# Performance work log

Measured on AMD Instinct MI355X. Metric: run time of the kernel, lower is better.

The kernel has to match this reference:

```python
import jax, jax.numpy as jnp
import numpy as np


def _u(k, shape, s):
    return jax.random.uniform(k, shape, jnp.float32, -s, s)


def setup_inputs() -> dict:
    B, T, F, H = 256, 256, 128, 256
    key = jax.random.key(0)
    ks = jax.random.split(key, 40)
    sH = 1.0 / np.sqrt(H).astype(np.float32)
    sF = 1.0 / np.sqrt(F).astype(np.float32)
    s2F = 1.0 / np.sqrt(2 * F).astype(np.float32)
    s3F = 1.0 / np.sqrt(3 * F).astype(np.float32)
    d = {
        'x': jax.random.normal(ks[0], (B, T, F), jnp.float32),
        'masking': (jax.random.uniform(ks[1], (B, T, F)) < 0.8).astype(jnp.float32),
        'time_lag': jax.random.uniform(ks[2], (B, T, F), jnp.float32),
        # forward LSTMCell (torch layout: W_ih [4H,2F], W_hh [4H,H], gates i,f,g,o)
        'fw_Wih': _u(ks[3], (4 * H, 2 * F), sH), 'fw_Whh': _u(ks[4], (4 * H, H), sH),
        'fw_bih': _u(ks[5], (4 * H,), sH), 'fw_bhh': _u(ks[6], (4 * H,), sH),
        'bw_Wih': _u(ks[7], (4 * H, 2 * F), sH), 'bw_Whh': _u(ks[8], (4 * H, H), sH),
        'bw_bih': _u(ks[9], (4 * H,), sH), 'bw_bhh': _u(ks[10], (4 * H,), sH),
        'fwlin_W': _u(ks[11], (F, H), sH), 'fwlin_b': _u(ks[12], (F,), sH),
        'bwlin_W': _u(ks[13], (F, H), sH), 'bwlin_b': _u(ks[14], (F,), sH),
        'fwz_W': _u(ks[15], (F, F), sF), 'fwz_b': _u(ks[16], (F,), sF),
        'bwz_W': _u(ks[17], (F, F), sF), 'bwz_b': _u(ks[18], (F,), sF),
        # beta linear 2F -> 3F
        'fwbeta_W': _u(ks[19], (3 * F, 2 * F), s2F), 'fwbeta_b': _u(ks[20], (3 * F,), s2F),
        'bwbeta_W': _u(ks[21], (3 * F, 2 * F), s2F), 'bwbeta_b': _u(ks[22], (3 * F,), s2F),
        # time-lag decay F -> H (both directions)
        'lag_W': _u(ks[23], (H, F), sF), 'lag_b': _u(ks[24], (H,), sF),
        'lagb_W': _u(ks[25], (H, F), sF), 'lagb_b': _u(ks[26], (H,), sF),
        # r_beta H -> F (both directions)
        'rbeta_W': _u(ks[27], (F, H), sH), 'rbeta_b': _u(ks[28], (F,), sH),
        'rbetab_W': _u(ks[29], (F, H), sH), 'rbetab_b': _u(ks[30], (F,), sH),
        # shared linear_layer_test 3F -> F
        'test_W': _u(ks[31], (F, 3 * F), s3F), 'test_b': _u(ks[32], (F,), s3F),
    }
    return d


def _lstm_cell(inp, h, c, Wih, Whh, bih, bhh):
    g = inp @ Wih.T + bih + h @ Whh.T + bhh
    i, f, gg, o = jnp.split(g, 4, axis=-1)
    c2 = jax.nn.sigmoid(f) * c + jax.nn.sigmoid(i) * jnp.tanh(gg)
    h2 = jax.nn.sigmoid(o) * jnp.tanh(c2)
    return h2, c2


def _run_dir(x, m, rr, rb, lin_W, lin_b, z_W, z_b, beta_W, beta_b, test_W, test_b, Wih, Whh, bih, bhh):
    # x, m: [T,B,F]; rr: [T,B,H]; rb: [T,B,F]
    F = x.shape[-1]
    offdiag = 1.0 - jnp.eye(F, dtype=x.dtype)

    def step(carry, inp):
        h, c = carry
        xj, mj, rj, rbj = inp
        out = h @ lin_W.T + lin_b                                 # [B,F]
        x_c = mj * xj + (1.0 - mj) * out
        z = x_c @ (z_W * offdiag).T + z_b
        beta = jax.nn.sigmoid(jnp.concatenate([mj, rbj], -1) @ beta_W.T + beta_b)
        beta = beta @ test_W.T + test_b                           # [B,F]
        c_val = beta * z + (1.0 - beta) * out
        c_c = mj * xj + (1.0 - mj) * c_val
        h2, c2 = _lstm_cell(jnp.concatenate([c_c, mj], -1), h * rj, c, Wih, Whh, bih, bhh)
        return (h2, c2), (out, z, c_val)

    bs, H = x.shape[1], Whh.shape[-1]
    h0 = jnp.zeros((bs, H), x.dtype)
    _, (outs, zs, cs) = jax.lax.scan(step, (h0, h0), (x, m, rr, rb))
    return outs, zs, cs


def reference(x, masking, time_lag, fw_Wih, fw_Whh, fw_bih, fw_bhh, bw_Wih, bw_Whh, bw_bih, bw_bhh, fwlin_W, fwlin_b, bwlin_W, bwlin_b, fwz_W, fwz_b, bwz_W, bwz_b, fwbeta_W, fwbeta_b, bwbeta_W, bwbeta_b, lag_W, lag_b, lagb_W, lagb_b, rbeta_W, rbeta_b, rbetab_W, rbetab_b, test_W, test_b):
    xt = jnp.transpose(x, (1, 0, 2))         # [T,B,F]
    mt = jnp.transpose(masking, (1, 0, 2))
    lt = jnp.transpose(time_lag, (1, 0, 2))
    # forward direction decay
    rr_f = jnp.exp(-jax.nn.relu(lt @ lag_W.T + lag_b))            # [T,B,H]
    rb_f = rr_f @ rbeta_W.T + rbeta_b                             # [T,B,F]
    of, zf, cf = _run_dir(xt, mt, rr_f, rb_f, fwlin_W, fwlin_b, fwz_W, fwz_b,
                          fwbeta_W, fwbeta_b, test_W, test_b, fw_Wih, fw_Whh, fw_bih, fw_bhh)
    # backward direction: iterate time reversed, then un-reverse outputs
    rr_b = jnp.exp(-jax.nn.relu(lt @ lagb_W.T + lagb_b))
    rb_b = rr_b @ rbetab_W.T + rbetab_b
    rev = lambda a: a[::-1]
    ob, zb, cb = _run_dir(rev(xt), rev(mt), rev(rr_b), rev(rb_b), bwlin_W, bwlin_b,
                          bwz_W, bwz_b, bwbeta_W, bwbeta_b, test_W, test_b,
                          bw_Wih, bw_Whh, bw_bih, bw_bhh)
    ob, zb, cb = rev(ob), rev(zb), rev(cb)
    perm = lambda a: jnp.transpose(a, (1, 0, 2))                  # back to [B,T,F]
    return (perm(of), perm(zf), perm(cf), perm(ob), perm(zb), perm(cb))
```

## Files before the change

kernel.cpp:

```cpp
#include <hip/hip_runtime.h>
#include <stdint.h>

#define TT 256
#define FF 128
#define HH 256
#define BB 256
#define BTc (BB * TT)
#define BTFc ((size_t)BB * TT * FF)

typedef __attribute__((ext_vector_type(8))) short short8;
typedef __attribute__((ext_vector_type(4))) float floatx4;
typedef __attribute__((ext_vector_type(4))) int intx4;

__device__ __forceinline__ floatx4 mfma16(short8 a, short8 b, floatx4 c) {
    return __builtin_amdgcn_mfma_f32_16x16x32_bf16(a, b, c, 0, 0, 0);
}
__device__ __forceinline__ intx4 mfmai8(long a, long b, intx4 c) {
    return __builtin_amdgcn_mfma_i32_16x16x32_i8(a, b, c, 0, 0, 0);
}

__device__ __forceinline__ float bf2f(short s) {
    return __uint_as_float(((unsigned)(unsigned short)s) << 16);
}
__device__ __forceinline__ short f2bf(float f) {
    unsigned u = __float_as_uint(f);
    u += 0x7FFFu + ((u >> 16) & 1u);
    return (short)(u >> 16);
}
__device__ __forceinline__ short8 ld_cvt8(const float* __restrict__ p) {
    short8 r;
#pragma unroll
    for (int j = 0; j < 8; ++j) r[j] = f2bf(p[j]);
    return r;
}
__device__ __forceinline__ float sigf(float x) { return 1.f / (1.f + __expf(-x)); }
__device__ __forceinline__ float tanhf_(float x) { return 1.f - 2.f / (1.f + __expf(2.f * x)); }

#define BARSYNC() do { asm volatile("s_waitcnt lgkmcnt(0)" ::: "memory"); \
                       __builtin_amdgcn_s_barrier(); } while (0)

struct PrepArgs {
    const float *s0, *s1, *s2, *s3, *s4, *s5, *s6;
    short *d0, *d1, *d2, *d3, *d4, *d5, *d6;
};
struct ScaleDesc { const float* src; int stride; int coloff; int K; int nrows; int sbase; };
struct ScaleArgs { ScaleDesc d[6]; float* s; };
struct PackBDesc { const float* src; short* dst; int stride; int coloff; int kts; int diag; int groups; };
struct AArgs { PrepArgs p; ScaleArgs s; PackBDesc b[6]; };

__global__ __launch_bounds__(256) void k_a(AArgs A) {
    if (blockIdx.x < 1472) {
        int i = blockIdx.x * 256 + threadIdx.x;
        const PrepArgs& P = A.p;
        if (i < 32768) { P.d0[i] = f2bf(P.s0[i]); return; }  i -= 32768;
        if (i < 32768) { P.d1[i] = f2bf(P.s1[i]); return; }  i -= 32768;
        if (i < 32768) { P.d2[i] = f2bf(P.s2[i]); return; }  i -= 32768;
        if (i < 32768) { P.d3[i] = f2bf(P.s3[i]); return; }  i -= 32768;
        if (i < 98304) { P.d4[i] = f2bf(P.s4[i]); return; }  i -= 98304;
        if (i < 98304) { P.d5[i] = f2bf(P.s5[i]); return; }  i -= 98304;
        if (i < 49152) { P.d6[i] = f2bf(P.s6[i]); return; }
        return;
    }
    if (blockIdx.x < 2560) {
        int gw = ((blockIdx.x - 1472) * 256 + threadIdx.x) >> 6;
        int lane = threadIdx.x & 63;
#pragma unroll 1
        for (int i = 0; i < 6; ++i) {
            if (gw < A.s.d[i].nrows) {
                const float* p = A.s.d[i].src + (size_t)gw * A.s.d[i].stride + A.s.d[i].coloff;
                float amax = 0.f;
                for (int j = lane; j < A.s.d[i].K; j += 64) amax = fmaxf(amax, fabsf(p[j]));
#pragma unroll
                for (int off = 32; off; off >>= 1) amax = fmaxf(amax, __shfl_xor(amax, off, 64));
                if (lane == 0) A.s.s[A.s.d[i].sbase + gw] = fmaxf(amax, 1e-20f);
                return;
            }
            gw -= A.s.d[i].nrows;
        }
        return;
    }
    int g = (blockIdx.x - 2560) * 256 + threadIdx.x;
#pragma unroll 1
    for (int i = 0; i < 6; ++i) {
        const PackBDesc& D = A.b[i];
        if (g < D.groups) {
            int frag = g >> 6, lane = g & 63;
            int nt = frag >> 2, kt = frag & 3;
            int ln = lane & 15, q4 = lane >> 4;
            int row = nt * 16 + ln;
            const float* p = D.src + (size_t)row * D.stride + D.coloff + kt * 32 + q4 * 8;
            short* dp = D.dst + (size_t)g * 8;
#pragma unroll
            for (int j = 0; j < 8; ++j) {
                int col = kt * 32 + q4 * 8 + j;
                float v = p[j];
                if (D.diag && col == row) v = 0.f;
                dp[j] = f2bf(v);
            }
            return;
        }
        g -= D.groups;
    }
}

struct PackQDesc { const float* src; char* dst; int stride; int coloff; int kts; int sbase; int groups; };
struct BArgs {
    const float* lt;
    const short* lagW0; const float* lagb0; const short* rbW0; const float* rbb0;
    short* rr0; short* rb0;
    const short* lagW1; const float* lagb1; const short* rbW1; const float* rbb1;
    short* rr1; short* rb1;
    const float* m;
    const short* wmB0; const short* wmB1;
    short* gb0; short* gb1;
    PackQDesc q[4]; const float* s;
};

__global__ __launch_bounds__(256) void k_b(BArgs A) {
    __shared__ short rrS[128][264];
    const int tid = threadIdx.x, lane = tid & 63, w = tid >> 6;
    const int ln = lane & 15, q4 = lane >> 4;

    if (blockIdx.x < 1024) {
        int b = blockIdx.x;
        const int dir = b >> 9; b &= 511;
        const int tc  = b & 7;
        const int q4d = (b >> 3) & 3;
        const int bg  = b >> 5;
        const short* lagW = dir ? A.lagW1 : A.lagW0;
        const float* lagb = dir ? A.lagb1 : A.lagb0;
        const short* rbW  = dir ? A.rbW1  : A.rbW0;
        const float* rbb  = dir ? A.rbb1  : A.rbb0;
        short* rr = dir ? A.rr1 : A.rr0;
        short* rb = dir ? A.rb1 : A.rb0;

#pragma unroll
        for (int mt = 0; mt < 2; ++mt) {
            const int rbase = w * 32 + mt * 16;
            floatx4 acc[16];
#pragma unroll
            for (int nt = 0; nt < 16; ++nt) { floatx4 z = {0.f, 0.f, 0.f, 0.f}; acc[nt] = z; }
            const int r = rbase + ln;
            const size_t aoff = ((size_t)(bg * 16 + q4d * 4 + (r >> 5)) * TT + tc * 32 + (r & 31)) * FF;
#pragma unroll
            for (int kt = 0; kt < 4; ++kt) {
                short8 a = ld_cvt8(A.lt + aoff + kt * 32 + q4 * 8);
#pragma unroll
                for (int nt = 0; nt < 16; ++nt) {
                    short8 bfr = *(const short8*)(lagW + (nt * 16 + ln) * 128 + kt * 32 + q4 * 8);
                    acc[nt] = mfma16(a, bfr, acc[nt]);
                }
            }
#pragma unroll
            for (int nt = 0; nt < 16; ++nt) {
                int n = nt * 16 + ln;
                float bias = lagb[n];
#pragma unroll
                for (int r2 = 0; r2 < 4; ++r2) {
                    int row = rbase + q4 * 4 + r2;
                    rrS[row][n] = f2bf(__expf(-fmaxf(acc[nt][r2] + bias, 0.f)));
                }
            }
        }
        __syncthreads();
        for (int c = tid; c < 32 * 256; c += 256) {
            int tl = c >> 8, n = c & 255;
            unsigned long long pk =
                ((unsigned long long)(unsigned short)rrS[tl][n]) |
                ((unsigned long long)(unsigned short)rrS[32 + tl][n] << 16) |
                ((unsigned long long)(unsigned short)rrS[64 + tl][n] << 32) |
                ((unsigned long long)(unsigned short)rrS[96 + tl][n] << 48);
            size_t doff = ((((size_t)(bg * TT + tc * 32 + tl) * 16 + (n >> 4)) * 64)
                           + q4d * 16 + (n & 15)) * 4;
            *(unsigned long long*)(rr + doff) = pk;
        }
#pragma unroll
        for (int mt = 0; mt < 2; ++mt) {
            const int rbase = w * 32 + mt * 16;
            floatx4 acc[8];
#pragma unroll
            for (int nt = 0; nt < 8; ++nt) { floatx4 z = {0.f, 0.f, 0.f, 0.f}; acc[nt] = z; }
#pragma unroll
            for (int kt = 0; kt < 8; ++kt) {
                short8 a = *(const short8*)&rrS[rbase + ln][kt * 32 + q4 * 8];
#pragma unroll
                for (int nt = 0; nt < 8; ++nt) {
                    short8 bfr = *(const short8*)(rbW + (nt * 16 + ln) * 256 + kt * 32 + q4 * 8);
                    acc[nt] = mfma16(a, bfr, acc[nt]);
                }
            }
#pragma unroll
            for (int nt = 0; nt < 8; ++nt) {
                int n = nt * 16 + ln;
                float bias = rbb[n];
#pragma unroll
                for (int r2 = 0; r2 < 4; ++r2) {
                    int row = rbase + q4 * 4 + r2;
                    size_t roff = ((size_t)(bg * 16 + q4d * 4 + (row >> 5)) * TT
                                   + tc * 32 + (row & 31)) * 128;
                    rb[roff + n] = f2bf(acc[nt][r2] + bias);
                }
            }
        }
        return;
    }

    if (blockIdx.x < 3072) {
        int task = (blockIdx.x - 1024) * 4 + w;
        const int dir = task >> 12; task &= 4095;
        const int bg = task >> 8, t = task & 255;
        const short* wB = dir ? A.wmB1 : A.wmB0;
        short* gb = dir ? A.gb1 : A.gb0;

        short8 a[4];
#pragma unroll
        for (int kt = 0; kt < 4; ++kt)
            a[kt] = ld_cvt8(A.m + ((size_t)(bg * 16 + ln) * TT + t) * FF + kt * 32 + q4 * 8);

        short* dst = gb + (size_t)task * 16384 + lane * 4;
#pragma unroll 2
        for (int nt = 0; nt < 64; ++nt) {
            floatx4 acc = {0.f, 0.f, 0.f, 0.f};
#pragma unroll
            for (int kt = 0; kt < 4; ++kt) {
                short8 bfr = *(const short8*)(wB + (nt * 4 + kt) * 512 + lane * 8);
                acc = mfma16(a[kt], bfr, acc);
            }
            unsigned long long pk =
                ((unsigned long long)(unsigned short)f2bf(acc[0])) |
                ((unsigned long long)(unsigned short)f2bf(acc[1]) << 16) |
                ((unsigned long long)(unsigned short)f2bf(acc[2]) << 32) |
                ((unsigned long long)(unsigned short)f2bf(acc[3]) << 48);
            *(unsigned long long*)(dst + nt * 256) = pk;
        }
        return;
    }

    int g = (blockIdx.x - 3072) * 256 + tid;
#pragma unroll 1
    for (int i = 0; i < 4; ++i) {
        const PackQDesc& D = A.q[i];
        if (g < D.groups) {
            int frag = g >> 6, plane = g & 63;
            int nt = frag / D.kts, kt = frag - nt * D.kts;
            int pln = plane & 15, pq4 = plane >> 4;
            int row = nt * 16 + pln;
            const float* p = D.src + (size_t)row * D.stride + D.coloff + kt * 32 + pq4 * 8;
            float inv = 127.f / A.s[D.sbase + row];
            char* dp = D.dst + (size_t)g * 8;
#pragma unroll
            for (int j = 0; j < 8; ++j) {
                int q = __float2int_rn(p[j] * inv);
                q = q > 127 ? 127 : (q < -127 ? -127 : q);
                dp[j] = (char)q;
            }
            return;
        }
        g -= D.groups;
    }
}

__global__ __launch_bounds__(256) void k_beta2(
    const float* __restrict__ m,
    const short* __restrict__ rb0, const short* __restrict__ rb1,
    const short* __restrict__ bW0, const short* __restrict__ bW1,
    const float* __restrict__ bb0, const float* __restrict__ bb1,
    const short* __restrict__ tW, const float* __restrict__ tb,
    short* __restrict__ bout0, short* __restrict__ bout1) {
    __shared__ short uS[64][392];
    const int tid = threadIdx.x, lane = tid & 63, w = tid >> 6;
    const int ln = lane & 15, q4 = lane >> 4;
    const int dir = blockIdx.x >> 10;
    const size_t r0 = (size_t)(blockIdx.x & 1023) * 64;
    const short* rb = dir ? rb1 : rb0;
    const short* bW = dir ? bW1 : bW0;
    const float* bb = dir ? bb1 : bb0;
    short* bout = dir ? bout1 : bout0;
    const int rbase = w * 16;

    {
        floatx4 acc[24];
#pragma unroll
        for (int nt = 0; nt < 24; ++nt) { floatx4 z = {0.f, 0.f, 0.f, 0.f}; acc[nt] = z; }
#pragma unroll
        for (int kt = 0; kt < 8; ++kt) {
            short8 a;
            if (kt < 4) a = ld_cvt8(m + (r0 + rbase + ln) * 128 + kt * 32 + q4 * 8);
            else        a = *(const short8*)(rb + (r0 + rbase + ln) * 128 + (kt - 4) * 32 + q4 * 8);
#pragma unroll
            for (int nt = 0; nt < 24; ++nt) {
                short8 b = *(const short8*)(bW + (nt * 16 + ln) * 256 + kt * 32 + q4 * 8);
                acc[nt] = mfma16(a, b, acc[nt]);
            }
        }
#pragma unroll
        for (int nt = 0; nt < 24; ++nt) {
            int n = nt * 16 + ln;
            float bias = bb[n];
#pragma unroll
            for (int r = 0; r < 4; ++r)
                uS[rbase + q4 * 4 + r][n] = f2bf(sigf(acc[nt][r] + bias));
        }
    }
    __syncthreads();
    {
        floatx4 acc[8];
#pragma unroll
        for (int nt = 0; nt < 8; ++nt) { floatx4 z = {0.f, 0.f, 0.f, 0.f}; acc[nt] = z; }
#pragma unroll
        for (int kt = 0; kt < 12; ++kt) {
            short8 a = *(const short8*)&uS[rbase + ln][kt * 32 + q4 * 8];
#pragma unroll
            for (int nt = 0; nt < 8; ++nt) {
                short8 b = *(const short8*)(tW + (nt * 16 + ln) * 384 + kt * 32 + q4 * 8);
                acc[nt] = mfma16(a, b, acc[nt]);
            }
        }
#pragma unroll
        for (int nt = 0; nt < 8; ++nt) {
            int n = nt * 16 + ln;
            float bias = tb[n];
#pragma unroll
            for (int r = 0; r < 4; ++r)
                bout[(r0 + rbase + q4 * 4 + r) * 128 + n] = f2bf(acc[nt][r] + bias);
        }
    }
}

struct ScanArgs {
    const float* x; const float* m;
    const short* rr0; const short* rr1;
    const short* beta0; const short* beta1;
    const short* gb0; const short* gb1;
    const char* whh0; const char* whh1;
    const char* lin0; const char* lin1;
    const short* wihc0; const short* wihc1;
    const short* zw0; const short* zw1;
    const float* s_all;
    const float* bih0; const float* bhh0; const float* bih1; const float* bhh1;
    const float* linb0; const float* linb1; const float* zb0; const float* zb1;
    float* out;
};

__global__ __launch_bounds__(1024, 4) void k_scan(ScanArgs A) {
    const int tid = threadIdx.x;
    const int lane = tid & 63;
    const int w = tid >> 6;
    const int ln = lane & 15;
    const int q4 = lane >> 4;
    const int dir = blockIdx.x >> 4;
    const int bgi = blockIdx.x & 15;
    const int bg0 = bgi * 16;

    const short* rrF   = dir ? A.rr1   : A.rr0;
    const short* beta  = dir ? A.beta1 : A.beta0;
    const short* gbF   = dir ? A.gb1   : A.gb0;
    const char*  whhQ  = dir ? A.whh1  : A.whh0;
    const char*  linQ  = dir ? A.lin1  : A.lin0;
    const short* wihcB = dir ? A.wihc1 : A.wihc0;
    const short* zwB   = dir ? A.zw1   : A.zw0;
    const float* bih   = dir ? A.bih1  : A.bih0;
    const float* bhh   = dir ? A.bhh1  : A.bhh0;
    const float* linb  = dir ? A.linb1 : A.linb0;
    const float* zb    = dir ? A.zb1   : A.zb0;
    const int so_whh  = dir ? 1024 : 0;
    const int so_lin  = 4096 + (dir ? 128 : 0);

    __shared__ char  hS8[16][264];
    __shared__ char  hrS8[16][264];
    __shared__ char  msS8[16][136];
    __shared__ short xS[16][136];
    __shared__ short bS[16][136];
    __shared__ short outS[16][136];
    __shared__ short ccS[16][136];
    __shared__ short zwS[16384];
    __shared__ char  linS8[32768];

    long WhhP[4][8];
#pragma unroll
    for (int q = 0; q < 4; ++q)
#pragma unroll
        for (int kt = 0; kt < 8; ++kt)
            WhhP[q][kt] = *(const long*)(whhQ + (((w + 16 * q) * 8 + kt) * 512 + lane * 8));

    float fhh[4], gb[4];
#pragma unroll
    for (int q = 0; q < 4; ++q) {
        int n = (w + 16 * q) * 16 + ln;
        fhh[q] = A.s_all[so_whh + n] * (1.f / 16129.f);
        gb[q]  = bih[n] + bhh[n];
    }
    float flin = 0.f, lb;
    if (w < 8) { int n = w * 16 + ln; flin = A.s_all[so_lin + n] * (1.f / 16129.f); lb = linb[n]; }
    else       { lb = zb[(w - 8) * 16 + ln]; }

    for (int i = tid; i < 16384; i += 1024) zwS[i] = zwB[i];
    for (int i = tid; i < 4096; i += 1024) ((long*)linS8)[i] = ((const long*)linQ)[i];
    for (int i = tid; i < 16 * 264; i += 1024) { hS8[i / 264][i % 264] = 0; hrS8[i / 264][i % 264] = 0; }

    auto GATES = [&](floatx4 (&g)[4], const long (&gq)[4]) {
#pragma unroll
        for (int pass = 0; pass < 2; ++pass) {
            const int q0 = pass * 2, q1 = pass * 2 + 1;
            intx4 gi0 = {0, 0, 0, 0}, gi1 = {0, 0, 0, 0};
#pragma unroll
            for (int kt = 0; kt < 8; ++kt) {
                long hrf = *(const long*)&hrS8[ln][kt * 32 + q4 * 8];
                gi0 = mfmai8(hrf, WhhP[q0][kt], gi0);
                gi1 = mfmai8(hrf, WhhP[q1][kt], gi1);
            }
#pragma unroll
            for (int r = 0; r < 4; ++r) {
                g[q0][r] = (float)gi0[r] * fhh[q0]
                         + bf2f((short)(((unsigned long long)gq[q0]) >> (16 * r))) + gb[q0];
                g[q1][r] = (float)gi1[r] * fhh[q1]
                         + bf2f((short)(((unsigned long long)gq[q1]) >> (16 * r))) + gb[q1];
            }
        }
    };

    const int tfirst = dir ? (TT - 1) : 0;
    {
        float2 xf = *(const float2*)(A.x + ((size_t)(bg0 + w) * TT + tfirst) * FF + lane * 2);
        float2 mf2 = *(const float2*)(A.m + ((size_t)(bg0 + w) * TT + tfirst) * FF + lane * 2);
        int    bf = *(const int*)(beta + ((size_t)(bg0 + w) * TT + tfirst) * FF + lane * 2);
        xS[w][lane * 2 + 0] = f2bf(xf.x);
        xS[w][lane * 2 + 1] = f2bf(xf.y);
        *(int*)&bS[w][lane * 2] = bf;
        msS8[w][lane * 2 + 0] = (char)(mf2.x != 0.f);
        msS8[w][lane * 2 + 1] = (char)(mf2.y != 0.f);
    }
    long gq[4];
#pragma unroll
    for (int q = 0; q < 4; ++q)
        gq[q] = *(const long*)(gbF + (((size_t)(bgi * TT + tfirst) * 64) + (w + 16 * q)) * 256
                                     + lane * 4);
    floatx4 cfr = {0.f, 0.f, 0.f, 0.f};
    __syncthreads();

    for (int tt = 0; tt < TT; ++tt) {
        const int t = dir ? (TT - 1 - tt) : tt;
        const int tn = dir ? (t > 0 ? t - 1 : 0) : (t < TT - 1 ? t + 1 : t);
        const size_t rowoffn = ((size_t)(bg0 + w) * TT + tn) * FF;

        float2 x_nxt = *(const float2*)(A.x + rowoffn + lane * 2);
        float2 m_nxt = *(const float2*)(A.m + rowoffn + lane * 2);
        int    b_nxt = *(const int*)(beta + rowoffn + lane * 2);
        unsigned long long rrv = *(const unsigned long long*)
            (rrF + ((((size_t)(bgi * TT + tn) * 16 + w) * 64) + lane) * 4);

        floatx4 g[4];
        if (w >= 8) {
            GATES(g, gq);
        } else {
            intx4 oi = {0, 0, 0, 0};
#pragma unroll
            for (int kt = 0; kt < 8; ++kt) {
                long lf = *(const long*)&linS8[(w * 8 + kt) * 512 + lane * 8];
                long hf = *(const long*)&hS8[ln][kt * 32 + q4 * 8];
                oi = mfmai8(hf, lf, oi);
            }
#pragma unroll
            for (int r = 0; r < 4; ++r)
                outS[q4 * 4 + r][w * 16 + ln] = f2bf((float)oi[r] * flin + lb);
        }
        BARSYNC();

        if (w >= 8) {
            floatx4 zv = {lb, lb, lb, lb};
#pragma unroll
            for (int kt = 0; kt < 4; ++kt) {
                const int c8 = kt * 32 + q4 * 8;
                short8 xv = *(const short8*)&xS[ln][c8];
                short8 ov = *(const short8*)&outS[ln][c8];
                unsigned long long mv = *(const unsigned long long*)&msS8[ln][c8];
                short8 xc;
#pragma unroll
                for (int j = 0; j < 8; ++j)
                    xc[j] = ((mv >> (8 * j)) & 0xffULL) ? xv[j] : ov[j];
                short8 zf = *(const short8*)&zwS[((w - 8) * 4 + kt) * 512 + lane * 8];
                zv = mfma16(xc, zf, zv);
            }
#pragma unroll
            for (int r = 0; r < 4; ++r) {
                const int row = q4 * 4 + r, col = (w - 8) * 16 + ln;
                short z16 = f2bf(zv[r]);
                float z0 = bf2f(z16);
                float o  = bf2f(outS[row][col]);
                float b  = bf2f(bS[row][col]);
                float cv = b * z0 + (1.f - b) * o;
                ccS[row][col] = msS8[row][col] ? xS[row][col] : f2bf(cv);
                size_t ob = (size_t)dir * 3 * BTFc + ((size_t)(bg0 + row) * TT + t) * FF + col;
                A.out[ob + BTFc]     = z0;
                A.out[ob + 2 * BTFc] = cv;
            }
        } else {
            {
                const int orow = 2 * w + (lane >> 5);
                const int ocol = (lane & 31) * 4;
                long ov4 = *(const long*)&outS[orow][ocol];
                float4 vo;
                vo.x = bf2f((short)(ov4));
                vo.y = bf2f((short)(ov4 >> 16));
                vo.z = bf2f((short)(ov4 >> 32));
                vo.w = bf2f((short)(ov4 >> 48));
                size_t ob = (size_t)dir * 3 * BTFc + ((size_t)(bg0 + orow) * TT + t) * FF + ocol;
                *(float4*)(A.out + ob) = vo;
            }
            GATES(g, gq);
        }
        BARSYNC();

#pragma unroll
        for (int q = 0; q < 4; ++q)
            gq[q] = *(const long*)(gbF + (((size_t)(bgi * TT + tn) * 64) + (w + 16 * q)) * 256
                                         + lane * 4);
#pragma unroll
        for (int kt = 0; kt < 4; ++kt) {
            short8 ccf = *(const short8*)&ccS[ln][kt * 32 + q4 * 8];
#pragma unroll
            for (int q = 0; q < 4; ++q) {
                short8 wc = *(const short8*)(wihcB + ((w + 16 * q) * 4 + kt) * 512 + lane * 8);
                g[q] = mfma16(ccf, wc, g[q]);
            }
        }
#pragma unroll
        for (int r = 0; r < 4; ++r) {
            float gi_ = g[0][r], gf_ = g[1][r], gg_ = g[2][r], go_ = g[3][r];
            float c2 = sigf(gf_) * cfr[r] + sigf(gi_) * tanhf_(gg_);
            float h2 = sigf(go_) * tanhf_(c2);
            cfr[r] = c2;
            float rv = bf2f((short)(rrv >> (16 * r)));
            hS8[q4 * 4 + r][w * 16 + ln]  = (char)__float2int_rn(h2 * 127.f);
            hrS8[q4 * 4 + r][w * 16 + ln] = (char)__float2int_rn(h2 * rv * 127.f);
        }
        xS[w][lane * 2 + 0] = f2bf(x_nxt.x);
        xS[w][lane * 2 + 1] = f2bf(x_nxt.y);
        *(int*)&bS[w][lane * 2] = b_nxt;
        msS8[w][lane * 2 + 0] = (char)(m_nxt.x != 0.f);
        msS8[w][lane * 2 + 1] = (char)(m_nxt.y != 0.f);
        BARSYNC();
    }
}

extern "C" void kernel_launch(void* const* d_in, const int* in_sizes, int n_in,
                              void* d_out, int out_size, void* d_ws, size_t ws_size,
                              hipStream_t stream) {
    (void)in_sizes; (void)n_in; (void)out_size; (void)ws_size;
    const float* x        = (const float*)d_in[0];
    const float* m        = (const float*)d_in[1];
    const float* lt       = (const float*)d_in[2];
    const float* fw_Wih   = (const float*)d_in[3];
    const float* fw_Whh   = (const float*)d_in[4];
    const float* fw_bih   = (const float*)d_in[5];
    const float* fw_bhh   = (const float*)d_in[6];
    const float* bw_Wih   = (const float*)d_in[7];
    const float* bw_Whh   = (const float*)d_in[8];
    const float* bw_bih   = (const float*)d_in[9];
    const float* bw_bhh   = (const float*)d_in[10];
    const float* fwlin_W  = (const float*)d_in[11];
    const float* fwlin_b  = (const float*)d_in[12];
    const float* bwlin_W  = (const float*)d_in[13];
    const float* bwlin_b  = (const float*)d_in[14];
    const float* fwz_W    = (const float*)d_in[15];
    const float* fwz_b    = (const float*)d_in[16];
    const float* bwz_W    = (const float*)d_in[17];
    const float* bwz_b    = (const float*)d_in[18];
    const float* fwbeta_W = (const float*)d_in[19];
    const float* fwbeta_b = (const float*)d_in[20];
    const float* bwbeta_W = (const float*)d_in[21];
    const float* bwbeta_b = (const float*)d_in[22];
    const float* lag_W    = (const float*)d_in[23];
    const float* lag_b    = (const float*)d_in[24];
    const float* lagb_W   = (const float*)d_in[25];
    const float* lagb_b   = (const float*)d_in[26];
    const float* rbeta_W  = (const float*)d_in[27];
    const float* rbeta_b  = (const float*)d_in[28];
    const float* rbetab_W = (const float*)d_in[29];
    const float* rbetab_b = (const float*)d_in[30];
    const float* test_W   = (const float*)d_in[31];
    const float* test_b   = (const float*)d_in[32];

    char* ws = (char*)d_ws;
    size_t o = 0;
    auto alloc = [&](size_t bytes) { char* p = ws + o; o += (bytes + 255) & ~(size_t)255; return p; };
    short* lagW0b  = (short*)alloc(65536);
    short* lagW1b  = (short*)alloc(65536);
    short* rbW0b   = (short*)alloc(65536);
    short* rbW1b   = (short*)alloc(65536);
    short* betaW0b = (short*)alloc(196608);
    short* betaW1b = (short*)alloc(196608);
    short* testWb  = (short*)alloc(98304);
    float* s_all   = (float*)alloc(4352 * 4);
    char*  whhQ0   = (char*)alloc(262144);
    char*  whhQ1   = (char*)alloc(262144);
    char*  linQ0   = (char*)alloc(32768);
    char*  linQ1   = (char*)alloc(32768);
    short* wihcB0  = (short*)alloc(262144);
    short* wihcB1  = (short*)alloc(262144);
    short* wihmB0  = (short*)alloc(262144);
    short* wihmB1  = (short*)alloc(262144);
    short* zwB0    = (short*)alloc(32768);
    short* zwB1    = (short*)alloc(32768);
    o = (o + ((size_t)1 << 20) - 1) & ~(((size_t)1 << 20) - 1);
    short* rr0 = (short*)(ws + o); o += (size_t)BTc * 256 * 2;
    short* rr1 = (short*)(ws + o); o += (size_t)BTc * 256 * 2;
    short* rb0 = (short*)(ws + o); o += (size_t)BTc * 128 * 2;
    short* rb1 = (short*)(ws + o); o += (size_t)BTc * 128 * 2;
    short* bt0 = (short*)(ws + o); o += (size_t)BTc * 128 * 2;
    short* bt1 = (short*)(ws + o); o += (size_t)BTc * 128 * 2;
    short* gb0 = (short*)(ws + o); o += (size_t)BTc * 1024 * 2;
    short* gb1 = (short*)(ws + o); o += (size_t)BTc * 1024 * 2;

    AArgs aa;
    aa.p.s0 = lag_W;    aa.p.d0 = lagW0b;
    aa.p.s1 = lagb_W;   aa.p.d1 = lagW1b;
    aa.p.s2 = rbeta_W;  aa.p.d2 = rbW0b;
    aa.p.s3 = rbetab_W; aa.p.d3 = rbW1b;
    aa.p.s4 = fwbeta_W; aa.p.d4 = betaW0b;
    aa.p.s5 = bwbeta_W; aa.p.d5 = betaW1b;
    aa.p.s6 = test_W;   aa.p.d6 = testWb;
    aa.s.d[0] = { fw_Whh,  256, 0,   256, 1024, 0 };
    aa.s.d[1] = { bw_Whh,  256, 0,   256, 1024, 1024 };
    aa.s.d[2] = { fw_Wih,  256, 128, 128, 1024, 2048 };
    aa.s.d[3] = { bw_Wih,  256, 128, 128, 1024, 3072 };
    aa.s.d[4] = { fwlin_W, 256, 0,   256, 128,  4096 };
    aa.s.d[5] = { bwlin_W, 256, 0,   256, 128,  4224 };
    aa.s.s = s_all;
    aa.b[0] = { fw_Wih, wihcB0, 256, 0,   4, 0, 16384 };
    aa.b[1] = { bw_Wih, wihcB1, 256, 0,   4, 0, 16384 };
    aa.b[2] = { fwz_W,  zwB0,   128, 0,   4, 1, 2048 };
    aa.b[3] = { bwz_W,  zwB1,   128, 0,   4, 1, 2048 };
    aa.b[4] = { fw_Wih, wihmB0, 256, 128, 4, 0, 16384 };
    aa.b[5] = { bw_Wih, wihmB1, 256, 128, 4, 0, 16384 };
    k_a<<<2832, 256, 0, stream>>>(aa);

    BArgs bb;
    bb.lt = lt;
    bb.lagW0 = lagW0b; bb.lagb0 = lag_b;  bb.rbW0 = rbW0b; bb.rbb0 = rbeta_b;
    bb.rr0 = rr0; bb.rb0 = rb0;
    bb.lagW1 = lagW1b; bb.lagb1 = lagb_b; bb.rbW1 = rbW1b; bb.rbb1 = rbetab_b;
    bb.rr1 = rr1; bb.rb1 = rb1;
    bb.m = m; bb.wmB0 = wihmB0; bb.wmB1 = wihmB1; bb.gb0 = gb0; bb.gb1 = gb1;
    bb.q[0] = { fw_Whh,  whhQ0,  256, 0,   8, 0,    32768 };
    bb.q[1] = { bw_Whh,  whhQ1,  256, 0,   8, 1024, 32768 };
    bb.q[2] = { fwlin_W, linQ0,  256, 0,   8, 4096, 4096 };
    bb.q[3] = { bwlin_W, linQ1,  256, 0,   8, 4224, 4096 };
    bb.s = s_all;
    k_b<<<3360, 256, 0, stream>>>(bb);

    k_beta2<<<2048, 256, 0, stream>>>(m, rb0, rb1, betaW0b, betaW1b,
                                      fwbeta_b, bwbeta_b, testWb, test_b, bt0, bt1);

    ScanArgs sa;
    sa.x = x; sa.m = m;
    sa.rr0 = rr0; sa.rr1 = rr1; sa.beta0 = bt0; sa.beta1 = bt1;
    sa.gb0 = gb0; sa.gb1 = gb1;
    sa.whh0 = whhQ0; sa.whh1 = whhQ1;
    sa.lin0 = linQ0; sa.lin1 = linQ1;
    sa.wihc0 = wihcB0; sa.wihc1 = wihcB1;
    sa.zw0 = zwB0; sa.zw1 = zwB1;
    sa.s_all = s_all;
    sa.bih0 = fw_bih; sa.bhh0 = fw_bhh; sa.bih1 = bw_bih; sa.bhh1 = bw_bhh;
    sa.linb0 = fwlin_b; sa.linb1 = bwlin_b; sa.zb0 = fwz_b; sa.zb1 = bwz_b;
    sa.out = (float*)d_out;
    k_scan<<<32, 1024, 0, stream>>>(sa);
}
```

Before: 4.919 ms.

## Regroup prep kernels to co-schedule independent work and shrink beta GEMM tiles

Splits the small lag and r_beta weight conversion into its own tiny kernel. The remaining weight prep (bf16 conversion, scale computation, B packing) is merged into the kernel that computes the decay terms, and the beta/test GEMM is merged with the gate precompute and quantized packing. The beta GEMM now uses 32-row blocks split across four waves, with fewer accumulators per wave. The goal is to overlap independent prep work, cut launches and raise occupancy. It keeps four kernel launches and changes the block decomposition.

```diff
diff --git a/kernel.cpp b/kernel.cpp
--- a/kernel.cpp
+++ b/kernel.cpp
@@ -39,84 +39,34 @@
 #define BARSYNC() do { asm volatile("s_waitcnt lgkmcnt(0)" ::: "memory"); \
                        __builtin_amdgcn_s_barrier(); } while (0)
 
-struct PrepArgs {
-    const float *s0, *s1, *s2, *s3, *s4, *s5, *s6;
-    short *d0, *d1, *d2, *d3, *d4, *d5, *d6;
-};
+__global__ __launch_bounds__(256) void k_p0(
+    const float* __restrict__ s0, const float* __restrict__ s1,
+    const float* __restrict__ s2, const float* __restrict__ s3,
+    short* __restrict__ d0, short* __restrict__ d1,
+    short* __restrict__ d2, short* __restrict__ d3) {
+    int i = blockIdx.x * 256 + threadIdx.x;
+    if (i < 32768) { d0[i] = f2bf(s0[i]); return; }  i -= 32768;
+    if (i < 32768) { d1[i] = f2bf(s1[i]); return; }  i -= 32768;
+    if (i < 32768) { d2[i] = f2bf(s2[i]); return; }
+    i -= 32768;
+    d3[i] = f2bf(s3[i]);
+}
+
 struct ScaleDesc { const float* src; int stride; int coloff; int K; int nrows; int sbase; };
 struct ScaleArgs { ScaleDesc d[6]; float* s; };
 struct PackBDesc { const float* src; short* dst; int stride; int coloff; int kts; int diag; int groups; };
-struct AArgs { PrepArgs p; ScaleArgs s; PackBDesc b[6]; };
-
-__global__ __launch_bounds__(256) void k_a(AArgs A) {
-    if (blockIdx.x < 1472) {
-        int i = blockIdx.x * 256 + threadIdx.x;
-        const PrepArgs& P = A.p;
-        if (i < 32768) { P.d0[i] = f2bf(P.s0[i]); return; }  i -= 32768;
-        if (i < 32768) { P.d1[i] = f2bf(P.s1[i]); return; }  i -= 32768;
-        if (i < 32768) { P.d2[i] = f2bf(P.s2[i]); return; }  i -= 32768;
-        if (i < 32768) { P.d3[i] = f2bf(P.s3[i]); return; }  i -= 32768;
-        if (i < 98304) { P.d4[i] = f2bf(P.s4[i]); return; }  i -= 98304;
-        if (i < 98304) { P.d5[i] = f2bf(P.s5[i]); return; }  i -= 98304;
-        if (i < 49152) { P.d6[i] = f2bf(P.s6[i]); return; }
-        return;
-    }
-    if (blockIdx.x < 2560) {
-        int gw = ((blockIdx.x - 1472) * 256 + threadIdx.x) >> 6;
-        int lane = threadIdx.x & 63;
-#pragma unroll 1
-        for (int i = 0; i < 6; ++i) {
-            if (gw < A.s.d[i].nrows) {
-                const float* p = A.s.d[i].src + (size_t)gw * A.s.d[i].stride + A.s.d[i].coloff;
-                float amax = 0.f;
-                for (int j = lane; j < A.s.d[i].K; j += 64) amax = fmaxf(amax, fabsf(p[j]));
-#pragma unroll
-                for (int off = 32; off; off >>= 1) amax = fmaxf(amax, __shfl_xor(amax, off, 64));
-                if (lane == 0) A.s.s[A.s.d[i].sbase + gw] = fmaxf(amax, 1e-20f);
-                return;
-            }
-            gw -= A.s.d[i].nrows;
-        }
-        return;
-    }
-    int g = (blockIdx.x - 2560) * 256 + threadIdx.x;
-#pragma unroll 1
-    for (int i = 0; i < 6; ++i) {
-        const PackBDesc& D = A.b[i];
-        if (g < D.groups) {
-            int frag = g >> 6, lane = g & 63;
-            int nt = frag >> 2, kt = frag & 3;
-            int ln = lane & 15, q4 = lane >> 4;
-            int row = nt * 16 + ln;
-            const float* p = D.src + (size_t)row * D.stride + D.coloff + kt * 32 + q4 * 8;
-            short* dp = D.dst + (size_t)g * 8;
-#pragma unroll
-            for (int j = 0; j < 8; ++j) {
-                int col = kt * 32 + q4 * 8 + j;
-                float v = p[j];
-                if (D.diag && col == row) v = 0.f;
-                dp[j] = f2bf(v);
-            }
-            return;
-        }
-        g -= D.groups;
-    }
-}
-
-struct PackQDesc { const float* src; char* dst; int stride; int coloff; int kts; int sbase; int groups; };
-struct BArgs {
+struct AArgs {
     const float* lt;
     const short* lagW0; const float* lagb0; const short* rbW0; const float* rbb0;
     short* rr0; short* rb0;
     const short* lagW1; const float* lagb1; const short* rbW1; const float* rbb1;
     short* rr1; short* rb1;
-    const float* m;
-    const short* wmB0; const short* wmB1;
-    short* gb0; short* gb1;
-    PackQDesc q[4]; const float* s;
+    const float *ps0, *ps1, *ps2; short *pd0, *pd1, *pd2;
+    ScaleArgs s;
+    PackBDesc b[6];
 };
 
-__global__ __launch_bounds__(256) void k_b(BArgs A) {
+__global__ __launch_bounds__(256) void k_a(AArgs A) {
     __shared__ short rrS[128][264];
     const int tid = threadIdx.x, lane = tid & 63, w = tid >> 6;
     const int ln = lane & 15, q4 = lane >> 4;
@@ -205,8 +155,138 @@
         return;
     }
 
+    if (blockIdx.x < 1984) {
+        int i = (blockIdx.x - 1024) * 256 + tid;
+        if (i < 98304) { A.pd0[i] = f2bf(A.ps0[i]); return; }  i -= 98304;
+        if (i < 98304) { A.pd1[i] = f2bf(A.ps1[i]); return; }  i -= 98304;
+        if (i < 49152) { A.pd2[i] = f2bf(A.ps2[i]); return; }
+        return;
+    }
+
     if (blockIdx.x < 3072) {
-        int task = (blockIdx.x - 1024) * 4 + w;
+        int gw = ((blockIdx.x - 1984) * 256 + tid) >> 6;
+#pragma unroll 1
+        for (int i = 0; i < 6; ++i) {
+            if (gw < A.s.d[i].nrows) {
+                const float* p = A.s.d[i].src + (size_t)gw * A.s.d[i].stride + A.s.d[i].coloff;
+                float amax = 0.f;
+                for (int j = lane; j < A.s.d[i].K; j += 64) amax = fmaxf(amax, fabsf(p[j]));
+#pragma unroll
+                for (int off = 32; off; off >>= 1) amax = fmaxf(amax, __shfl_xor(amax, off, 64));
+                if (lane == 0) A.s.s[A.s.d[i].sbase + gw] = fmaxf(amax, 1e-20f);
+                return;
+            }
+            gw -= A.s.d[i].nrows;
+        }
+        return;
+    }
+
+    int g = (blockIdx.x - 3072) * 256 + tid;
+#pragma unroll 1
+    for (int i = 0; i < 6; ++i) {
+        const PackBDesc& D = A.b[i];
+        if (g < D.groups) {
+            int frag = g >> 6, plane = g & 63;
+            int nt = frag >> 2, kt = frag & 3;
+            int pln = plane & 15, pq4 = plane >> 4;
+            int row = nt * 16 + pln;
+            const float* p = D.src + (size_t)row * D.stride + D.coloff + kt * 32 + pq4 * 8;
+            short* dp = D.dst + (size_t)g * 8;
+#pragma unroll
+            for (int j = 0; j < 8; ++j) {
+                int col = kt * 32 + pq4 * 8 + j;
+                float v = p[j];
+                if (D.diag && col == row) v = 0.f;
+                dp[j] = f2bf(v);
+            }
+            return;
+        }
+        g -= D.groups;
+    }
+}
+
+struct PackQDesc { const float* src; char* dst; int stride; int coloff; int kts; int sbase; int groups; };
+struct CArgs {
+    const float* m;
+    const short* rb0; const short* rb1;
+    const short* bW0; const short* bW1;
+    const float* bb0; const float* bb1;
+    const short* tW; const float* tb;
+    short* bt0; short* bt1;
+    const short* wmB0; const short* wmB1;
+    short* gb0; short* gb1;
+    PackQDesc q[4]; const float* s;
+};
+
+__global__ __launch_bounds__(256) void k_c(CArgs A) {
+    __shared__ short uS[32][392];
+    const int tid = threadIdx.x, lane = tid & 63, w = tid >> 6;
+    const int ln = lane & 15, q4 = lane >> 4;
+
+    if (blockIdx.x < 4096) {
+        const int dir = blockIdx.x >> 11;
+        const size_t r0 = (size_t)(blockIdx.x & 2047) * 32;
+        const short* rb = dir ? A.rb1 : A.rb0;
+        const short* bW = dir ? A.bW1 : A.bW0;
+        const float* bb = dir ? A.bb1 : A.bb0;
+        short* bout = dir ? A.bt1 : A.bt0;
+        const int rt = w >> 1;
+        const int nh = w & 1;
+
+        {
+            floatx4 acc[12];
+#pragma unroll
+            for (int j = 0; j < 12; ++j) { floatx4 z = {0.f, 0.f, 0.f, 0.f}; acc[j] = z; }
+#pragma unroll
+            for (int kt = 0; kt < 8; ++kt) {
+                short8 a;
+                if (kt < 4) a = ld_cvt8(A.m + (r0 + rt * 16 + ln) * 128 + kt * 32 + q4 * 8);
+                else        a = *(const short8*)(rb + (r0 + rt * 16 + ln) * 128 + (kt - 4) * 32 + q4 * 8);
+#pragma unroll
+                for (int j = 0; j < 12; ++j) {
+                    int nt = nh * 12 + j;
+                    short8 b = *(const short8*)(bW + (nt * 16 + ln) * 256 + kt * 32 + q4 * 8);
+                    acc[j] = mfma16(a, b, acc[j]);
+                }
+            }
+#pragma unroll
+            for (int j = 0; j < 12; ++j) {
+                int n = (nh * 12 + j) * 16 + ln;
+                float bias = bb[n];
+#pragma unroll
+                for (int r = 0; r < 4; ++r)
+                    uS[rt * 16 + q4 * 4 + r][n] = f2bf(sigf(acc[j][r] + bias));
+            }
+        }
+        __syncthreads();
+        {
+            floatx4 acc[4];
+#pragma unroll
+            for (int j = 0; j < 4; ++j) { floatx4 z = {0.f, 0.f, 0.f, 0.f}; acc[j] = z; }
+#pragma unroll
+            for (int kt = 0; kt < 12; ++kt) {
+                short8 a = *(const short8*)&uS[rt * 16 + ln][kt * 32 + q4 * 8];
+#pragma unroll
+                for (int j = 0; j < 4; ++j) {
+                    int nt = nh * 4 + j;
+                    short8 b = *(const short8*)(A.tW + (nt * 16 + ln) * 384 + kt * 32 + q4 * 8);
+                    acc[j] = mfma16(a, b, acc[j]);
+                }
+            }
+#pragma unroll
+            for (int j = 0; j < 4; ++j) {
+                int n = (nh * 4 + j) * 16 + ln;
+                float bias = A.tb[n];
+#pragma unroll
+                for (int r = 0; r < 4; ++r)
+                    bout[(r0 + rt * 16 + q4 * 4 + r) * 128 + n] = f2bf(acc[j][r] + bias);
+            }
+        }
+        return;
+    }
+
+    if (blockIdx.x < 6144) {
+        int task = (blockIdx.x - 4096) * 4 + w;
         const int dir = task >> 12; task &= 4095;
         const int bg = task >> 8, t = task & 255;
         const short* wB = dir ? A.wmB1 : A.wmB0;
@@ -236,7 +316,7 @@
         return;
     }
 
-    int g = (blockIdx.x - 3072) * 256 + tid;
+    int g = (blockIdx.x - 6144) * 256 + tid;
 #pragma unroll 1
     for (int i = 0; i < 4; ++i) {
         const PackQDesc& D = A.q[i];
@@ -257,73 +337,6 @@
             return;
         }
         g -= D.groups;
-    }
-}
-
-__global__ __launch_bounds__(256) void k_beta2(
-    const float* __restrict__ m,
-    const short* __restrict__ rb0, const short* __restrict__ rb1,
-    const short* __restrict__ bW0, const short* __restrict__ bW1,
-    const float* __restrict__ bb0, const float* __restrict__ bb1,
-    const short* __restrict__ tW, const float* __restrict__ tb,
-    short* __restrict__ bout0, short* __restrict__ bout1) {
-    __shared__ short uS[64][392];
-    const int tid = threadIdx.x, lane = tid & 63, w = tid >> 6;
-    const int ln = lane & 15, q4 = lane >> 4;
-    const int dir = blockIdx.x >> 10;
-    const size_t r0 = (size_t)(blockIdx.x & 1023) * 64;
-    const short* rb = dir ? rb1 : rb0;
-    const short* bW = dir ? bW1 : bW0;
-    const float* bb = dir ? bb1 : bb0;
-    short* bout = dir ? bout1 : bout0;
-    const int rbase = w * 16;
-
-    {
-        floatx4 acc[24];
-#pragma unroll
-        for (int nt = 0; nt < 24; ++nt) { floatx4 z = {0.f, 0.f, 0.f, 0.f}; acc[nt] = z; }
-#pragma unroll
-        for (int kt = 0; kt < 8; ++kt) {
-            short8 a;
-            if (kt < 4) a = ld_cvt8(m + (r0 + rbase + ln) * 128 + kt * 32 + q4 * 8);
-            else        a = *(const short8*)(rb + (r0 + rbase + ln) * 128 + (kt - 4) * 32 + q4 * 8);
-#pragma unroll
-            for (int nt = 0; nt < 24; ++nt) {
-                short8 b = *(const short8*)(bW + (nt * 16 + ln) * 256 + kt * 32 + q4 * 8);
-                acc[nt] = mfma16(a, b, acc[nt]);
-            }
-        }
-#pragma unroll
-        for (int nt = 0; nt < 24; ++nt) {
-            int n = nt * 16 + ln;
-            float bias = bb[n];
-#pragma unroll
-            for (int r = 0; r < 4; ++r)
-                uS[rbase + q4 * 4 + r][n] = f2bf(sigf(acc[nt][r] + bias));
-        }
-    }
-    __syncthreads();
-    {
-        floatx4 acc[8];
-#pragma unroll
-        for (int nt = 0; nt < 8; ++nt) { floatx4 z = {0.f, 0.f, 0.f, 0.f}; acc[nt] = z; }
-#pragma unroll
-        for (int kt = 0; kt < 12; ++kt) {
-            short8 a = *(const short8*)&uS[rbase + ln][kt * 32 + q4 * 8];
-#pragma unroll
-            for (int nt = 0; nt < 8; ++nt) {
-                short8 b = *(const short8*)(tW + (nt * 16 + ln) * 384 + kt * 32 + q4 * 8);
-                acc[nt] = mfma16(a, b, acc[nt]);
-            }
-        }
-#pragma unroll
-        for (int nt = 0; nt < 8; ++nt) {
-            int n = nt * 16 + ln;
-            float bias = tb[n];
-#pragma unroll
-            for (int r = 0; r < 4; ++r)
-                bout[(r0 + rbase + q4 * 4 + r) * 128 + n] = f2bf(acc[nt][r] + bias);
-        }
     }
 }
 
@@ -612,14 +625,18 @@
     short* gb0 = (short*)(ws + o); o += (size_t)BTc * 1024 * 2;
     short* gb1 = (short*)(ws + o); o += (size_t)BTc * 1024 * 2;
 
+    k_p0<<<512, 256, 0, stream>>>(lag_W, lagb_W, rbeta_W, rbetab_W,
+                                  lagW0b, lagW1b, rbW0b, rbW1b);
+
     AArgs aa;
-    aa.p.s0 = lag_W;    aa.p.d0 = lagW0b;
-    aa.p.s1 = lagb_W;   aa.p.d1 = lagW1b;
-    aa.p.s2 = rbeta_W;  aa.p.d2 = rbW0b;
-    aa.p.s3 = rbetab_W; aa.p.d3 = rbW1b;
-    aa.p.s4 = fwbeta_W; aa.p.d4 = betaW0b;
-    aa.p.s5 = bwbeta_W; aa.p.d5 = betaW1b;
-    aa.p.s6 = test_W;   aa.p.d6 = testWb;
+    aa.lt = lt;
+    aa.lagW0 = lagW0b; aa.lagb0 = lag_b;  aa.rbW0 = rbW0b; aa.rbb0 = rbeta_b;
+    aa.rr0 = rr0; aa.rb0 = rb0;
+    aa.lagW1 = lagW1b; aa.lagb1 = lagb_b; aa.rbW1 = rbW1b; aa.rbb1 = rbetab_b;
+    aa.rr1 = rr1; aa.rb1 = rb1;
+    aa.ps0 = fwbeta_W; aa.pd0 = betaW0b;
+    aa.ps1 = bwbeta_W; aa.pd1 = betaW1b;
+    aa.ps2 = test_W;   aa.pd2 = testWb;
     aa.s.d[0] = { fw_Whh,  256, 0,   256, 1024, 0 };
     aa.s.d[1] = { bw_Whh,  256, 0,   256, 1024, 1024 };
     aa.s.d[2] = { fw_Wih,  256, 128, 128, 1024, 2048 };
@@ -633,24 +650,23 @@
     aa.b[3] = { bwz_W,  zwB1,   128, 0,   4, 1, 2048 };
     aa.b[4] = { fw_Wih, wihmB0, 256, 128, 4, 0, 16384 };
     aa.b[5] = { bw_Wih, wihmB1, 256, 128, 4, 0, 16384 };
-    k_a<<<2832, 256, 0, stream>>>(aa);
-
-    BArgs bb;
-    bb.lt = lt;
-    bb.lagW0 = lagW0b; bb.lagb0 = lag_b;  bb.rbW0 = rbW0b; bb.rbb0 = rbeta_b;
-    bb.rr0 = rr0; bb.rb0 = rb0;
-    bb.lagW1 = lagW1b; bb.lagb1 = lagb_b; bb.rbW1 = rbW1b; bb.rbb1 = rbetab_b;
-    bb.rr1 = rr1; bb.rb1 = rb1;
-    bb.m = m; bb.wmB0 = wihmB0; bb.wmB1 = wihmB1; bb.gb0 = gb0; bb.gb1 = gb1;
-    bb.q[0] = { fw_Whh,  whhQ0,  256, 0,   8, 0,    32768 };
-    bb.q[1] = { bw_Whh,  whhQ1,  256, 0,   8, 1024, 32768 };
-    bb.q[2] = { fwlin_W, linQ0,  256, 0,   8, 4096, 4096 };
-    bb.q[3] = { bwlin_W, linQ1,  256, 0,   8, 4224, 4096 };
-    bb.s = s_all;
-    k_b<<<3360, 256, 0, stream>>>(bb);
-
-    k_beta2<<<2048, 256, 0, stream>>>(m, rb0, rb1, betaW0b, betaW1b,
-                                      fwbeta_b, bwbeta_b, testWb, test_b, bt0, bt1);
+    k_a<<<3344, 256, 0, stream>>>(aa);
+
+    CArgs cc;
+    cc.m = m;
+    cc.rb0 = rb0; cc.rb1 = rb1;
+    cc.bW0 = betaW0b; cc.bW1 = betaW1b;
+    cc.bb0 = fwbeta_b; cc.bb1 = bwbeta_b;
+    cc.tW = testWb; cc.tb = test_b;
+    cc.bt0 = bt0; cc.bt1 = bt1;
+    cc.wmB0 = wihmB0; cc.wmB1 = wihmB1;
+    cc.gb0 = gb0; cc.gb1 = gb1;
+    cc.q[0] = { fw_Whh,  whhQ0,  256, 0,   8, 0,    32768 };
+    cc.q[1] = { bw_Whh,  whhQ1,  256, 0,   8, 1024, 32768 };
+    cc.q[2] = { fwlin_W, linQ0,  256, 0,   8, 4096, 4096 };
+    cc.q[3] = { bwlin_W, linQ1,  256, 0,   8, 4224, 4096 };
+    cc.s = s_all;
+    k_c<<<6432, 256, 0, stream>>>(cc);
 
     ScanArgs sa;
     sa.x = x; sa.m = m;
```

Result: faster. 4.773 ms (-3.0%).
